# Optimization experiments

Hardware: AMD Instinct MI355X
Metric: run time of the kernel (lower is better)

Reference implementation:

```python
import jax, jax.numpy as jnp
import numpy as np

N_NODES = 50000
N_EDGES = 800000
IN_DIM = 256
HID = 128


def setup_inputs() -> dict:
    key = jax.random.key(0)
    ks = jax.random.split(key, 8)
    x = jax.random.normal(ks[0], (N_NODES, IN_DIM), dtype=jnp.float32)
    edge_index = jax.random.randint(ks[1], (2, N_EDGES), 0, N_NODES, dtype=jnp.int32)
    edge_weight = jax.random.uniform(ks[2], (N_EDGES,), dtype=jnp.float32)
    # xavier_normal with gain=1.414 as in torch init
    g = 1.414
    W1 = jax.random.normal(ks[3], (HID, IN_DIM), dtype=jnp.float32) * (g * np.sqrt(2.0 / (HID + IN_DIM)))
    W2 = jax.random.normal(ks[4], (HID, HID), dtype=jnp.float32) * (g * np.sqrt(2.0 / (HID + HID)))
    b1 = jnp.zeros((HID,), dtype=jnp.float32)
    b2 = jnp.zeros((HID,), dtype=jnp.float32)
    a1 = jnp.full((1,), 0.25, dtype=jnp.float32)  # nn.PReLU() default init
    a2 = jnp.full((1,), 0.25, dtype=jnp.float32)
    return {"x": x, "edge_index": edge_index, "edge_weight": edge_weight,
            "W1": W1, "b1": b1, "a1": a1, "W2": W2, "b2": b2, "a2": a2}


def _gcn_layer(z, W, b, a, src, dst, w):
    # linear (no bias): [N, out]
    fts = z @ W.T
    # spmm: out[dst] += w * fts[src]
    msg = fts[src] * w[:, None]                      # [E, out]
    out = jax.ops.segment_sum(msg, dst, num_segments=N_NODES) + b
    # PReLU (single shared parameter)
    return jnp.where(out >= 0, out, a * out)


def reference(x, edge_index, edge_weight, W1, b1, a1, W2, b2, a2):
    src, dst = edge_index[0], edge_index[1]
    z = _gcn_layer(x, W1, b1, a1, src, dst, edge_weight)
    z = _gcn_layer(z, W2, b2, a2, src, dst, edge_weight)
    return z
```

## Files before the change

### kernel.cpp

```cpp
#include <hip/hip_runtime.h>
#include <hip/hip_bf16.h>

#define HID 128
#define BSH 6
#define BSZ 64
#define NBMAX 1024
#define HB 64
#define STAGE_BLKS 128

typedef unsigned int uint;
typedef unsigned short ushort;
typedef __attribute__((ext_vector_type(8))) short short8;
typedef __attribute__((ext_vector_type(4))) float f32x4;

__device__ __forceinline__ ushort bf16_of(float x) {
    return __bfloat16_as_ushort(__float2bfloat16(x));
}

__device__ __forceinline__ uint pack_bf16x2(float a, float b) {
    return (uint)bf16_of(a) | ((uint)bf16_of(b) << 16);
}

union FragAB { uint4 u; short8 s; };

__global__ __launch_bounds__(256) void pack_hist(
    const float* __restrict__ W1, const float* __restrict__ W2,
    ushort* __restrict__ Wb1, ushort* __restrict__ Wb2,
    const int* __restrict__ dst, int* __restrict__ hpart, int E, int NB) {
    int blk = blockIdx.x;
    if (blk >= 24) {
        __shared__ int h[NBMAX];
        int hb = blk - 24;
        for (int i = threadIdx.x; i < NB; i += 256) h[i] = 0;
        __syncthreads();
        int chunk = (E + HB - 1) / HB;
        int c0 = hb * chunk;
        int c1 = min(c0 + chunk, E);
        for (int e = c0 + threadIdx.x; e < c1; e += 256)
            atomicAdd(&h[dst[e] >> BSH], 1);
        __syncthreads();
        for (int i = threadIdx.x; i < NB; i += 256) hpart[hb * NBMAX + i] = h[i];
        return;
    }
    const float* W = (blk < 16) ? W1 : W2;
    ushort* Wb = (blk < 16) ? Wb1 : Wb2;
    int K = (blk < 16) ? 256 : 128;
    int t = ((blk < 16) ? blk : blk - 16) * 256 + threadIdx.x;
    int lane = t & 63, f = t >> 6;
    int s = f >> 3, c = f & 7;
    int m = c * 16 + (lane & 15);
    int k0 = s * 32 + (lane >> 4) * 8;
    const float* wr = W + (size_t)m * K + k0;
    float4 a = *(const float4*)wr;
    float4 b = *(const float4*)(wr + 4);
    uint4 o = make_uint4(pack_bf16x2(a.x, a.y), pack_bf16x2(a.z, a.w),
                         pack_bf16x2(b.x, b.y), pack_bf16x2(b.z, b.w));
    *(uint4*)(Wb + (size_t)t * 8) = o;
}

template <int K, bool ABF16>
__device__ __forceinline__ void gemm_body(
    const void* __restrict__ Xv, const ushort* __restrict__ Wb,
    ushort* __restrict__ out, int N, int bid) {
    const int lane = threadIdx.x & 63;
    const int wid  = threadIdx.x >> 6;
    const int n0   = bid * 64 + wid * 16;
    const int arow = n0 + (lane & 15);
    const bool ok  = arow < N;
    const int kgrp = (lane >> 4) * 8;
    constexpr int NS = K / 32;

    FragAB af[NS];
    if (ABF16) {
        const ushort* xr = (const ushort*)Xv + (size_t)arow * K + kgrp;
#pragma unroll
        for (int s = 0; s < NS; ++s)
            af[s].u = ok ? *(const uint4*)(xr + s * 32) : make_uint4(0, 0, 0, 0);
    } else {
        const float* xr = (const float*)Xv + (size_t)arow * K + kgrp;
        float4 xa[NS], xb[NS];
#pragma unroll
        for (int s = 0; s < NS; ++s) {
            xa[s] = ok ? *(const float4*)(xr + s * 32) : make_float4(0.f, 0.f, 0.f, 0.f);
            xb[s] = ok ? *(const float4*)(xr + s * 32 + 4) : make_float4(0.f, 0.f, 0.f, 0.f);
        }
#pragma unroll
        for (int s = 0; s < NS; ++s)
            af[s].u = make_uint4(pack_bf16x2(xa[s].x, xa[s].y), pack_bf16x2(xa[s].z, xa[s].w),
                                 pack_bf16x2(xb[s].x, xb[s].y), pack_bf16x2(xb[s].z, xb[s].w));
    }

    f32x4 acc[8];
#pragma unroll
    for (int c = 0; c < 8; ++c) acc[c] = (f32x4){0.f, 0.f, 0.f, 0.f};

#pragma unroll
    for (int s = 0; s < NS; ++s) {
#pragma unroll
        for (int c = 0; c < 8; ++c) {
            FragAB bfr;
            bfr.u = *(const uint4*)(Wb + (size_t)((s * 8 + c) * 64 + lane) * 8);
            acc[c] = __builtin_amdgcn_mfma_f32_16x16x32_bf16(af[s].s, bfr.s, acc[c], 0, 0, 0);
        }
    }
    const int col = lane & 15;
    const int rb = n0 + (lane >> 4) * 4;
#pragma unroll
    for (int c = 0; c < 8; ++c) {
#pragma unroll
        for (int r = 0; r < 4; ++r) {
            int n = rb + r;
            if (n < N) out[(size_t)n * HID + c * 16 + col] = bf16_of(acc[c][r]);
        }
    }
}

__device__ __forceinline__ void stage_body(
    const int* __restrict__ src, const int* __restrict__ dst,
    const float* __restrict__ w, int* __restrict__ gcur,
    int2* __restrict__ staged, int E, int NB, int bid) {
    __shared__ int lh[NBMAX], lb[NBMAX];
    for (int i = threadIdx.x; i < NB; i += 256) lh[i] = 0;
    __syncthreads();
    int chunk = (E + STAGE_BLKS - 1) / STAGE_BLKS;
    int c0 = bid * chunk;
    int c1 = min(c0 + chunk, E);
    for (int e = c0 + threadIdx.x; e < c1; e += 256)
        atomicAdd(&lh[dst[e] >> BSH], 1);
    __syncthreads();
    for (int i = threadIdx.x; i < NB; i += 256) {
        int c = lh[i];
        lb[i] = c ? atomicAdd(&gcur[i], c) : 0;
        lh[i] = 0;
    }
    __syncthreads();
    for (int e = c0 + threadIdx.x; e < c1; e += 256) {
        int d = dst[e];
        int b = d >> BSH;
        int slot = lb[b] + atomicAdd(&lh[b], 1);
        staged[slot] = make_int2(src[e] | ((d & (BSZ - 1)) << 16), __float_as_int(w[e]));
    }
}

__global__ __launch_bounds__(256, 2) void gemm1_stage(
    const float* __restrict__ X, const ushort* __restrict__ Wb1,
    ushort* __restrict__ fts, int N, int gblk,
    const int* __restrict__ src, const int* __restrict__ dst,
    const float* __restrict__ w, int* __restrict__ gcur,
    int2* __restrict__ staged, int E, int NB) {
    int bid = blockIdx.x;
    if (bid < gblk) {
        gemm_body<256, false>(X, Wb1, fts, N, bid);
    } else {
        stage_body(src, dst, w, gcur, staged, E, NB, bid - gblk);
    }
}

template <int K, bool ABF16>
__global__ __launch_bounds__(256, 2) void gemm_mfma(
    const void* __restrict__ Xv, const ushort* __restrict__ Wb,
    ushort* __restrict__ out, int N) {
    gemm_body<K, ABF16>(Xv, Wb, out, N, blockIdx.x);
}

__global__ __launch_bounds__(NBMAX) void bucket_scan(const int* __restrict__ hpart,
                                                     int* __restrict__ gbase,
                                                     int* __restrict__ gcur, int NB, int E) {
    __shared__ int l[NBMAX];
    int t = threadIdx.x;
    int v = 0;
    if (t < NB)
        for (int b = 0; b < HB; ++b) v += hpart[b * NBMAX + t];
    l[t] = v;
    __syncthreads();
    int x = v;
    for (int o = 1; o < NBMAX; o <<= 1) {
        int y = (t >= o) ? l[t - o] : 0;
        __syncthreads();
        x += y;
        l[t] = x;
        __syncthreads();
    }
    if (t < NB) { gbase[t] = x - v; gcur[t] = x - v; }
    if (t == 0) gbase[NB] = E;
}

__global__ __launch_bounds__(256) void node_sort(
    const int* __restrict__ gbase, const int2* __restrict__ staged,
    int2* __restrict__ csr, int* __restrict__ off, int N) {
    __shared__ int hist[BSZ];
    __shared__ int cur[BSZ];
    const int b = blockIdx.x;
    const int s0 = gbase[b], s1 = gbase[b + 1];
    const int t = threadIdx.x;
    if (t < BSZ) hist[t] = 0;
    __syncthreads();
    for (int e = s0 + t; e < s1; e += 256)
        atomicAdd(&hist[(staged[e].x >> 16) & (BSZ - 1)], 1);
    __syncthreads();
    if (t < BSZ) {
        int x = hist[t];
        int incl = x;
#pragma unroll
        for (int o = 1; o < BSZ; o <<= 1) {
            int y = __shfl_up(incl, o, BSZ);
            if (t >= o) incl += y;
        }
        int excl = incl - x;
        cur[t] = excl;
        int n = (b << BSH) + t;
        if (n <= N) off[n] = s0 + excl;
    }
    __syncthreads();
    for (int e = s0 + t; e < s1; e += 256) {
        int2 m = staged[e];
        int d = (m.x >> 16) & (BSZ - 1);
        int p = atomicAdd(&cur[d], 1);
        csr[s0 + p] = m;
    }
}

template <bool OUTBF16>
__global__ __launch_bounds__(256) void csr_gather_bf16(
    const int* __restrict__ off, const int2* __restrict__ edges,
    const ushort* __restrict__ fts, void* __restrict__ outv,
    const float* __restrict__ bias, const float* __restrict__ alpha, int N) {
    int d = blockIdx.x * 4 + (threadIdx.x >> 6);
    if (d >= N) return;
    const int lane = threadIdx.x & 63;
    const int g = lane >> 4;
    const int sub = lane & 15;
    int p = off[d];
    const int end = off[d + 1];
    float acc[8];
#pragma unroll
    for (int j = 0; j < 8; ++j) acc[j] = 0.f;

#define LOBITS(u_) __uint_as_float((u_) << 16)
#define HIBITS(u_) __uint_as_float((u_) & 0xffff0000u)
#define ROWOF(M_) (*(const uint4*)(fts + (size_t)((M_).x & 0xffff) * HID + sub * 8))
#define ACC8(R_, W_)                                              \
    do {                                                          \
        acc[0] += (W_) * LOBITS((R_).x); acc[1] += (W_) * HIBITS((R_).x); \
        acc[2] += (W_) * LOBITS((R_).y); acc[3] += (W_) * HIBITS((R_).y); \
        acc[4] += (W_) * LOBITS((R_).z); acc[5] += (W_) * HIBITS((R_).z); \
        acc[6] += (W_) * LOBITS((R_).w); acc[7] += (W_) * HIBITS((R_).w); \
    } while (0)

    for (; p + 16 <= end; p += 16) {
        int2 m0 = edges[p + g], m1 = edges[p + 4 + g];
        int2 m2 = edges[p + 8 + g], m3 = edges[p + 12 + g];
        uint4 r0 = ROWOF(m0), r1 = ROWOF(m1), r2 = ROWOF(m2), r3 = ROWOF(m3);
        float w0 = __int_as_float(m0.y), w1 = __int_as_float(m1.y);
        float w2 = __int_as_float(m2.y), w3 = __int_as_float(m3.y);
        ACC8(r0, w0); ACC8(r1, w1); ACC8(r2, w2); ACC8(r3, w3);
    }
    for (; p + 8 <= end; p += 8) {
        int2 ma = edges[p + g];
        int2 mb = edges[p + 4 + g];
        uint4 ra = ROWOF(ma), rb = ROWOF(mb);
        float wa = __int_as_float(ma.y), wb = __int_as_float(mb.y);
        ACC8(ra, wa);
        ACC8(rb, wb);
    }
    for (; p < end; p += 4) {
        int i = p + g;
        int2 m = edges[(i < end) ? i : (end - 1)];
        float wt = (i < end) ? __int_as_float(m.y) : 0.f;
        uint4 r = ROWOF(m);
        ACC8(r, wt);
    }
#undef ACC8
#undef ROWOF
#undef LOBITS
#undef HIBITS

#pragma unroll
    for (int j = 0; j < 8; ++j) {
        acc[j] += __shfl_xor(acc[j], 16);
        acc[j] += __shfl_xor(acc[j], 32);
    }

    const float a = alpha[0];
#pragma unroll
    for (int j = 0; j < 8; ++j) {
        float v = acc[j] + bias[sub * 8 + j];
        acc[j] = v >= 0.f ? v : a * v;
    }
    if (g == 0) {
        if (OUTBF16) {
            uint4 o = make_uint4(pack_bf16x2(acc[0], acc[1]), pack_bf16x2(acc[2], acc[3]),
                                 pack_bf16x2(acc[4], acc[5]), pack_bf16x2(acc[6], acc[7]));
            *(uint4*)((ushort*)outv + (size_t)d * HID + sub * 8) = o;
        } else {
            float* op = (float*)outv + (size_t)d * HID + sub * 8;
            *(float4*)op = make_float4(acc[0], acc[1], acc[2], acc[3]);
            *(float4*)(op + 4) = make_float4(acc[4], acc[5], acc[6], acc[7]);
        }
    }
}

extern "C" void kernel_launch(void* const* d_in, const int* in_sizes, int n_in,
                              void* d_out, int out_size, void* d_ws, size_t ws_size,
                              hipStream_t stream) {
    const float* x  = (const float*)d_in[0];
    const int*   ei = (const int*)d_in[1];
    const float* ew = (const float*)d_in[2];
    const float* W1 = (const float*)d_in[3];
    const float* b1 = (const float*)d_in[4];
    const float* a1 = (const float*)d_in[5];
    const float* W2 = (const float*)d_in[6];
    const float* b2 = (const float*)d_in[7];
    const float* a2 = (const float*)d_in[8];
    float* out = (float*)d_out;

    int N = in_sizes[0] / 256;
    int E = in_sizes[2];
    const int* src = ei;
    const int* dst = ei + E;
    int NB = (N + BSZ - 1) >> BSH;

    ushort* fts    = (ushort*)d_ws;
    ushort* agg    = fts + (size_t)N * HID;
    int2*   staged = (int2*)(agg + (size_t)N * HID);
    int2*   csr    = staged + E;
    ushort* Wb1    = (ushort*)(csr + E);
    ushort* Wb2    = Wb1 + 128 * 256;
    int*    hpart  = (int*)(Wb2 + 128 * 128);
    int*    gbase  = hpart + HB * NBMAX;
    int*    gcur   = gbase + NBMAX + 1;
    int*    off    = gcur + NBMAX;

    int gblk = (N + 63) / 64;
    int ggrid = (N + 3) / 4;

    pack_hist<<<24 + HB, 256, 0, stream>>>(W1, W2, Wb1, Wb2, dst, hpart, E, NB);
    bucket_scan<<<1, NBMAX, 0, stream>>>(hpart, gbase, gcur, NB, E);
    gemm1_stage<<<gblk + STAGE_BLKS, 256, 0, stream>>>(
        x, Wb1, fts, N, gblk, src, dst, ew, gcur, staged, E, NB);
    node_sort<<<NB, 256, 0, stream>>>(gbase, staged, csr, off, N);
    csr_gather_bf16<true><<<ggrid, 256, 0, stream>>>(off, csr, fts, agg, b1, a1, N);
    gemm_mfma<128, true><<<gblk, 256, 0, stream>>>(agg, Wb2, fts, N);
    csr_gather_bf16<false><<<ggrid, 256, 0, stream>>>(off, csr, fts, out, b2, a2, N);
}
```

Baseline: 144.7 us.

## Precompute per-block bucket offsets in scan, drop second histogram pass in staging

The histogram kernel's per-block partial counts are now aligned with the staging blocks (HB equals STAGE_BLKS). The scan kernel computes an exclusive offset for every (block, bucket) pair, so each staging block can scatter directly without re-histogramming its edge chunk or doing global atomics on bucket cursors. This removes one pass over dst and a global atomic phase from the staging blocks. In exchange the single-block scan does more serial work per thread (128 reads and writes each) and the pbase buffer adds traffic.

```diff
diff --git a/kernel.cpp b/kernel.cpp
--- a/kernel.cpp
+++ b/kernel.cpp
@@ -5,8 +5,8 @@
 #define BSH 6
 #define BSZ 64
 #define NBMAX 1024
-#define HB 64
-#define STAGE_BLKS 128
+#define HB 128
+#define STAGE_BLKS HB
 
 typedef unsigned int uint;
 typedef unsigned short ushort;
@@ -117,23 +117,18 @@
 
 __device__ __forceinline__ void stage_body(
     const int* __restrict__ src, const int* __restrict__ dst,
-    const float* __restrict__ w, int* __restrict__ gcur,
+    const float* __restrict__ w, const int* __restrict__ pbase,
     int2* __restrict__ staged, int E, int NB, int bid) {
-    __shared__ int lh[NBMAX], lb[NBMAX];
-    for (int i = threadIdx.x; i < NB; i += 256) lh[i] = 0;
+    __shared__ int lh[NBMAX];
+    __shared__ int lb[NBMAX];
+    for (int i = threadIdx.x; i < NB; i += 256) {
+        lh[i] = 0;
+        lb[i] = pbase[bid * NBMAX + i];
+    }
     __syncthreads();
     int chunk = (E + STAGE_BLKS - 1) / STAGE_BLKS;
     int c0 = bid * chunk;
     int c1 = min(c0 + chunk, E);
-    for (int e = c0 + threadIdx.x; e < c1; e += 256)
-        atomicAdd(&lh[dst[e] >> BSH], 1);
-    __syncthreads();
-    for (int i = threadIdx.x; i < NB; i += 256) {
-        int c = lh[i];
-        lb[i] = c ? atomicAdd(&gcur[i], c) : 0;
-        lh[i] = 0;
-    }
-    __syncthreads();
     for (int e = c0 + threadIdx.x; e < c1; e += 256) {
         int d = dst[e];
         int b = d >> BSH;
@@ -146,13 +141,13 @@
     const float* __restrict__ X, const ushort* __restrict__ Wb1,
     ushort* __restrict__ fts, int N, int gblk,
     const int* __restrict__ src, const int* __restrict__ dst,
-    const float* __restrict__ w, int* __restrict__ gcur,
+    const float* __restrict__ w, const int* __restrict__ pbase,
     int2* __restrict__ staged, int E, int NB) {
     int bid = blockIdx.x;
     if (bid < gblk) {
         gemm_body<256, false>(X, Wb1, fts, N, bid);
     } else {
-        stage_body(src, dst, w, gcur, staged, E, NB, bid - gblk);
+        stage_body(src, dst, w, pbase, staged, E, NB, bid - gblk);
     }
 }
 
@@ -165,15 +160,19 @@
 
 __global__ __launch_bounds__(NBMAX) void bucket_scan(const int* __restrict__ hpart,
                                                      int* __restrict__ gbase,
-                                                     int* __restrict__ gcur, int NB, int E) {
+                                                     int* __restrict__ pbase, int NB, int E) {
     __shared__ int l[NBMAX];
     int t = threadIdx.x;
-    int v = 0;
-    if (t < NB)
-        for (int b = 0; b < HB; ++b) v += hpart[b * NBMAX + t];
-    l[t] = v;
-    __syncthreads();
-    int x = v;
+    int run = 0;
+    if (t < NB) {
+        for (int b = 0; b < HB; ++b) {
+            pbase[b * NBMAX + t] = run;
+            run += hpart[b * NBMAX + t];
+        }
+    }
+    l[t] = run;
+    __syncthreads();
+    int x = run;
     for (int o = 1; o < NBMAX; o <<= 1) {
         int y = (t >= o) ? l[t - o] : 0;
         __syncthreads();
@@ -181,7 +180,11 @@
         l[t] = x;
         __syncthreads();
     }
-    if (t < NB) { gbase[t] = x - v; gcur[t] = x - v; }
+    int excl = x - run;
+    if (t < NB) {
+        gbase[t] = excl;
+        for (int b = 0; b < HB; ++b) pbase[b * NBMAX + t] += excl;
+    }
     if (t == 0) gbase[NB] = E;
 }
 
@@ -327,17 +330,17 @@
     ushort* Wb1    = (ushort*)(csr + E);
     ushort* Wb2    = Wb1 + 128 * 256;
     int*    hpart  = (int*)(Wb2 + 128 * 128);
-    int*    gbase  = hpart + HB * NBMAX;
-    int*    gcur   = gbase + NBMAX + 1;
-    int*    off    = gcur + NBMAX;
+    int*    pbase  = hpart + HB * NBMAX;
+    int*    gbase  = pbase + HB * NBMAX;
+    int*    off    = gbase + NBMAX + 1;
 
     int gblk = (N + 63) / 64;
     int ggrid = (N + 3) / 4;
 
     pack_hist<<<24 + HB, 256, 0, stream>>>(W1, W2, Wb1, Wb2, dst, hpart, E, NB);
-    bucket_scan<<<1, NBMAX, 0, stream>>>(hpart, gbase, gcur, NB, E);
+    bucket_scan<<<1, NBMAX, 0, stream>>>(hpart, gbase, pbase, NB, E);
     gemm1_stage<<<gblk + STAGE_BLKS, 256, 0, stream>>>(
-        x, Wb1, fts, N, gblk, src, dst, ew, gcur, staged, E, NB);
+        x, Wb1, fts, N, gblk, src, dst, ew, pbase, staged, E, NB);
     node_sort<<<NB, 256, 0, stream>>>(gbase, staged, csr, off, N);
     csr_gather_bf16<true><<<ggrid, 256, 0, stream>>>(off, csr, fts, agg, b1, a1, N);
     gemm_mfma<128, true><<<gblk, 256, 0, stream>>>(agg, Wb2, fts, N);
```

Measured after the change: 158.1 us. +9.2%, slower.
